# Kernel tuning notes

Hardware: AMD Instinct MI355X
Metric: run time of the kernel (lower is better)

Reference implementation:

```python
import jax, jax.numpy as jnp
import numpy as np

B, L, D, H = 4, 1024, 1024, 16
HD = D // H  # head_dim = 64


def setup_inputs() -> dict:
    key = jax.random.key(0)
    k1, k2, k3, k4 = jax.random.split(key, 4)
    x = jax.random.normal(k1, (B, L, D), dtype=jnp.float32)
    # causal mask: positions where mask == 0 are filled with -inf
    mask = jnp.tril(jnp.ones((L, L), dtype=bool))[None, None, :, :]  # [1,1,L,L]
    w_qkv = jax.random.normal(k2, (D, 3 * D), dtype=jnp.float32) * (D ** -0.5)
    w_out = jax.random.normal(k3, (D, D), dtype=jnp.float32) * (D ** -0.5)
    rel_pos_bias = jax.random.normal(k4, (H, L, L), dtype=jnp.float32) * 0.02
    return {"x": x, "mask": mask, "w_qkv": w_qkv, "w_out": w_out,
            "rel_pos_bias": rel_pos_bias}


def reference(x, mask, w_qkv, w_out, rel_pos_bias):
    b, l, d = x.shape
    scale = HD ** -0.5
    qkv = (x @ w_qkv).reshape(b, l, 3, H, HD)          # [B,L,3,H,hd]
    q, k, v = qkv[:, :, 0], qkv[:, :, 1], qkv[:, :, 2]  # each [B,L,H,hd]
    # scores: [B,H,Lq,Lk]
    scores = jnp.einsum('bqhd,bkhd->bhqk', q, k) * scale
    scores = scores + rel_pos_bias[None, :, :l, :l]
    scores = jnp.where(mask, scores, -jnp.inf)
    attn = jax.nn.softmax(scores, axis=-1)  # dropout is identity in eval
    out = jnp.einsum('bhqk,bkhd->bqhd', attn, v).reshape(b, l, d)
    return out @ w_out
```

## Files before the change

### kernel.cpp

```cpp
#include <hip/hip_runtime.h>
#include <hip/hip_bf16.h>
#include <math.h>

#define B_  4
#define L_  1024
#define D_  1024
#define H_  16
#define HD_ 64
#define SCALE 0.125f
#define LOG2E 1.44269504f
#define SCALE_L2E (0.125f * 1.44269504f)
#define NEG_BIG -3.0e38f

typedef __bf16 bf16x8 __attribute__((ext_vector_type(8)));
typedef float  f32x4  __attribute__((ext_vector_type(4)));

__device__ __forceinline__ float b2f(unsigned short u) {
    union { unsigned int i; float f; } x; x.i = ((unsigned)u) << 16; return x.f;
}
__device__ __forceinline__ unsigned short f2b(float f) {
    __hip_bfloat16 h = __float2bfloat16(f);
    return *reinterpret_cast<unsigned short*>(&h);
}
__device__ __forceinline__ void gl_lds16(const void* g, void* l) {
    __builtin_amdgcn_global_load_lds(
        (const __attribute__((address_space(1))) void*)g,
        (__attribute__((address_space(3))) void*)l, 16, 0, 0);
}

__global__ __launch_bounds__(256) void prep_kernel(
    const float* __restrict__ x, const float* __restrict__ w_qkv,
    const float* __restrict__ w_out, unsigned short* __restrict__ xb,
    unsigned short* __restrict__ wqkvT, unsigned short* __restrict__ woutT)
{
    const int bid = blockIdx.x;
    if (bid < 4096) {
        int i = (bid * 256 + threadIdx.x) * 4;
        float4 v = *(const float4*)&x[i];
        ushort4 o = make_ushort4(f2b(v.x), f2b(v.y), f2b(v.z), f2b(v.w));
        *(ushort4*)&xb[i] = o;
        return;
    }
    __shared__ float tile[32][33];
    const float* w; unsigned short* wt; int N, n0, k0;
    if (bid < 7168) {
        int b2 = bid - 4096;
        w = w_qkv; wt = wqkvT; N = 3072;
        n0 = (b2 % 96) * 32; k0 = (b2 / 96) * 32;
    } else {
        int b3 = bid - 7168;
        w = w_out; wt = woutT; N = 1024;
        n0 = (b3 % 32) * 32; k0 = (b3 / 32) * 32;
    }
    const int tx = threadIdx.x & 31, ty = threadIdx.x >> 5;
#pragma unroll
    for (int i = 0; i < 4; i++) {
        int kk = ty + i * 8;
        tile[kk][tx] = w[(size_t)(k0 + kk) * N + n0 + tx];
    }
    __syncthreads();
#pragma unroll
    for (int i = 0; i < 4; i++) {
        int nn = ty + i * 8;
        wt[(size_t)(n0 + nn) * 1024 + k0 + tx] = f2b(tile[tx][nn]);
    }
}

__device__ __forceinline__ void gemm_core(
    const unsigned short* __restrict__ A, const unsigned short* __restrict__ Bt,
    unsigned short* As, unsigned short* Bs,
    int m0, int n0, int wave, int lane, int wm, int wn,
    f32x4 acc[4][4])
{
    const int srow = lane >> 2, spos = lane & 3;
    const int sc   = spos ^ ((srow >> 1) & 3);
    const int mlane = lane & 15, chunk = lane >> 4;
    const int foff  = mlane * 32 + (chunk ^ ((mlane >> 1) & 3)) * 8;

    for (int k0 = 0; k0 < 1024; k0 += 32) {
#pragma unroll
        for (int t = 0; t < 2; t++) {
            int rb = wave * 32 + t * 16;
            int r  = rb + srow;
            gl_lds16(&A [(size_t)(m0 + r) * 1024 + k0 + sc * 8], &As[rb * 32]);
            gl_lds16(&Bt[(size_t)(n0 + r) * 1024 + k0 + sc * 8], &Bs[rb * 32]);
        }
        __syncthreads();
        bf16x8 af[4], bfr[4];
#pragma unroll
        for (int i = 0; i < 4; i++) {
            af[i]  = *(const bf16x8*)&As[(wm * 64 + i * 16) * 32 + foff];
            bfr[i] = *(const bf16x8*)&Bs[(wn * 64 + i * 16) * 32 + foff];
        }
#pragma unroll
        for (int i = 0; i < 4; i++)
#pragma unroll
            for (int j = 0; j < 4; j++)
                acc[i][j] = __builtin_amdgcn_mfma_f32_16x16x32_bf16(
                    bfr[i], af[j], acc[i][j], 0, 0, 0);
        __syncthreads();
    }
}

__global__ __launch_bounds__(256) void qkv_gemm_kernel(
    const unsigned short* __restrict__ A, const unsigned short* __restrict__ Bt,
    unsigned short* __restrict__ qb, unsigned short* __restrict__ kb,
    unsigned short* __restrict__ vtb)
{
    __shared__ unsigned short As[128 * 32];
    __shared__ unsigned short Bs[128 * 32];
    const int tid  = threadIdx.x;
    const int wave = tid >> 6, lane = tid & 63;
    const int quad = lane >> 4, l16 = lane & 15;
    const int wm = wave >> 1, wn = wave & 1;
    const int m0 = blockIdx.y * 128, n0 = blockIdx.x * 128;
    f32x4 acc[4][4] = {};
    gemm_core(A, Bt, As, Bs, m0, n0, wave, lane, wm, wn, acc);

    const int s = n0 >> 10;
#pragma unroll
    for (int i = 0; i < 4; i++) {
        int n_base = n0 + wn * 64 + i * 16 + quad * 4;
        int h = (n_base >> 6) & 15, hd0 = n_base & 63;
#pragma unroll
        for (int j = 0; j < 4; j++) {
            int m = m0 + wm * 64 + j * 16 + l16;
            int b = m >> 10, l = m & 1023;
            if (s == 2) {
#pragma unroll
                for (int r = 0; r < 4; r++)
                    vtb[((size_t)((b * 16 + h) * 64 + hd0 + r)) * 1024 + l] =
                        f2b(acc[i][j][r]);
            } else {
                unsigned short* dst = (s == 0) ? qb : kb;
                unsigned short tmp[4];
#pragma unroll
                for (int r = 0; r < 4; r++) tmp[r] = f2b(acc[i][j][r]);
                *(ushort4*)&dst[(((size_t)(b * 16 + h) * 1024 + l) << 6) + hd0] =
                    *(ushort4*)tmp;
            }
        }
    }
}

__global__ __launch_bounds__(256) void out_gemm_kernel(
    const unsigned short* __restrict__ A, const unsigned short* __restrict__ Bt,
    float* __restrict__ out)
{
    __shared__ unsigned short As[128 * 32];
    __shared__ unsigned short Bs[64 * 32];
    const int tid  = threadIdx.x;
    const int wave = tid >> 6, lane = tid & 63;
    const int quad = lane >> 4, l16 = lane & 15;
    const int srow = lane >> 2, spos = lane & 3;
    const int sc   = spos ^ ((srow >> 1) & 3);
    const int mlane = lane & 15, chunk = lane >> 4;
    const int foff  = mlane * 32 + (chunk ^ ((mlane >> 1) & 3)) * 8;
    const int m0 = blockIdx.y * 128, n0 = blockIdx.x * 64;
    f32x4 acc[4][2] = {};

    for (int k0 = 0; k0 < 1024; k0 += 32) {
#pragma unroll
        for (int t = 0; t < 2; t++) {
            int rb = wave * 32 + t * 16;
            gl_lds16(&A[(size_t)(m0 + rb + srow) * 1024 + k0 + sc * 8], &As[rb * 32]);
        }
        {
            int rb = wave * 16;
            gl_lds16(&Bt[(size_t)(n0 + rb + srow) * 1024 + k0 + sc * 8], &Bs[rb * 32]);
        }
        __syncthreads();
        bf16x8 af[2], bfr[4];
#pragma unroll
        for (int i = 0; i < 2; i++)
            af[i]  = *(const bf16x8*)&As[(wave * 32 + i * 16) * 32 + foff];
#pragma unroll
        for (int j = 0; j < 4; j++)
            bfr[j] = *(const bf16x8*)&Bs[(j * 16) * 32 + foff];
#pragma unroll
        for (int jn = 0; jn < 4; jn++)
#pragma unroll
            for (int im = 0; im < 2; im++)
                acc[jn][im] = __builtin_amdgcn_mfma_f32_16x16x32_bf16(
                    bfr[jn], af[im], acc[jn][im], 0, 0, 0);
        __syncthreads();
    }
#pragma unroll
    for (int jn = 0; jn < 4; jn++) {
        int n_base = n0 + jn * 16 + quad * 4;
#pragma unroll
        for (int im = 0; im < 2; im++) {
            int m = m0 + wave * 32 + im * 16 + l16;
            float4 o = make_float4(acc[jn][im][0], acc[jn][im][1],
                                   acc[jn][im][2], acc[jn][im][3]);
            *(float4*)&out[(size_t)m * 1024 + n_base] = o;
        }
    }
}

__global__ __launch_bounds__(256, 2) void attn_mfma_kernel(
    const unsigned short* __restrict__ qb, const unsigned short* __restrict__ kb,
    const unsigned short* __restrict__ vtb, const float* __restrict__ bias,
    unsigned short* __restrict__ ob)
{
    __shared__ unsigned short Ks [2 * 64 * 72];
    __shared__ unsigned short Vts[2 * 64 * 72];
    __shared__ unsigned short Ps [128 * 72];

    const int tid  = threadIdx.x;
    const int wave = tid >> 6, lane = tid & 63;
    const int quad = lane >> 4, l16 = lane & 15;
    const int bh = blockIdx.x, b = bh >> 4, h = bh & 15;
    const int jlo = blockIdx.y;
    const int jhi = 15 - jlo;
    const int ktmax = jhi;
    const int srow = tid >> 3, scol = (tid & 7) * 8;
    const size_t qkv_base = (size_t)bh * (1024 * 64);

    const int qH  = jhi * 64 + wave * 16;
    const int qL  = jlo * 64 + wave * 16;
    const int qgH = qH + quad * 4;
    const int qgL = qL + quad * 4;

    bf16x8 aH0 = *(const bf16x8*)&qb[qkv_base + (size_t)(qH + l16) * 64 + quad * 8];
    bf16x8 aH1 = *(const bf16x8*)&qb[qkv_base + (size_t)(qH + l16) * 64 + 32 + quad * 8];
    bf16x8 aL0 = *(const bf16x8*)&qb[qkv_base + (size_t)(qL + l16) * 64 + quad * 8];
    bf16x8 aL1 = *(const bf16x8*)&qb[qkv_base + (size_t)(qL + l16) * 64 + 32 + quad * 8];

    uint4 kpre0 = *(const uint4*)&kb [qkv_base + (size_t)srow * 64 + scol];
    uint4 kpre1 = *(const uint4*)&kb [qkv_base + (size_t)(srow + 32) * 64 + scol];
    uint4 vpre0 = *(const uint4*)&vtb[qkv_base + (size_t)srow * 1024 + scol];
    uint4 vpre1 = *(const uint4*)&vtb[qkv_base + (size_t)(srow + 32) * 1024 + scol];

    float bA[16], bB[16];
#pragma unroll
    for (int nt = 0; nt < 4; nt++)
#pragma unroll
        for (int r = 0; r < 4; r++)
            bA[nt * 4 + r] =
                bias[((size_t)h * 1024 + qgH + r) * 1024 + nt * 16 + l16] * LOG2E;

    float lrH[4] = {}, lrL[4] = {};
    f32x4 OH[4] = {}, OL[4] = {};

    *(uint4*)&Ks [srow * 72 + scol]        = kpre0;
    *(uint4*)&Ks [(srow + 32) * 72 + scol] = kpre1;
    *(uint4*)&Vts[srow * 72 + scol]        = vpre0;
    *(uint4*)&Vts[(srow + 32) * 72 + scol] = vpre1;
    __syncthreads();

    auto strip = [&](int kt, const bf16x8& a0, const bf16x8& a1, const float* bc,
                     int qg, int psrow, f32x4* O, float* lr, bool dg) {
        const unsigned short* Kc = &Ks [(kt & 1) * 4608];
        const unsigned short* Vc = &Vts[(kt & 1) * 4608];
        f32x4 sacc[4] = {};
        __builtin_amdgcn_s_setprio(1);
#pragma unroll
        for (int nt = 0; nt < 4; nt++) {
            bf16x8 k0 = *(const bf16x8*)&Kc[(nt * 16 + l16) * 72 + quad * 8];
            bf16x8 k1 = *(const bf16x8*)&Kc[(nt * 16 + l16) * 72 + 32 + quad * 8];
            sacc[nt] = __builtin_amdgcn_mfma_f32_16x16x32_bf16(a0, k0, sacc[nt], 0, 0, 0);
            sacc[nt] = __builtin_amdgcn_mfma_f32_16x16x32_bf16(a1, k1, sacc[nt], 0, 0, 0);
        }
        __builtin_amdgcn_s_setprio(0);
#pragma unroll
        for (int nt = 0; nt < 4; nt++) {
            const int kg = kt * 64 + nt * 16 + l16;
#pragma unroll
            for (int r = 0; r < 4; r++) {
                float v = fmaf(sacc[nt][r], SCALE_L2E, bc[nt * 4 + r]);
                if (dg && kg > qg + r) v = NEG_BIG;
                float p = exp2f(v);
                lr[r] += p;
                Ps[(psrow + quad * 4 + r) * 72 + nt * 16 + l16] = f2b(p);
            }
        }
        bf16x8 p0 = *(const bf16x8*)&Ps[(psrow + l16) * 72 + quad * 8];
        bf16x8 p1 = *(const bf16x8*)&Ps[(psrow + l16) * 72 + 32 + quad * 8];
        __builtin_amdgcn_s_setprio(1);
#pragma unroll
        for (int dt = 0; dt < 4; dt++) {
            bf16x8 v0 = *(const bf16x8*)&Vc[(dt * 16 + l16) * 72 + quad * 8];
            bf16x8 v1 = *(const bf16x8*)&Vc[(dt * 16 + l16) * 72 + 32 + quad * 8];
            O[dt] = __builtin_amdgcn_mfma_f32_16x16x32_bf16(p0, v0, O[dt], 0, 0, 0);
            O[dt] = __builtin_amdgcn_mfma_f32_16x16x32_bf16(p1, v1, O[dt], 0, 0, 0);
        }
        __builtin_amdgcn_s_setprio(0);
    };

    auto tile = [&](int kt, float* bc, float* bn) {
        const bool pf = (kt < ktmax);
        if (pf) {
            const int kn = (kt + 1) * 64;
            kpre0 = *(const uint4*)&kb [qkv_base + (size_t)(kn + srow) * 64 + scol];
            kpre1 = *(const uint4*)&kb [qkv_base + (size_t)(kn + srow + 32) * 64 + scol];
            vpre0 = *(const uint4*)&vtb[qkv_base + (size_t)srow * 1024 + kn + scol];
            vpre1 = *(const uint4*)&vtb[qkv_base + (size_t)(srow + 32) * 1024 + kn + scol];
            const float* bp = &bias[((size_t)h * 1024 + qgH) * 1024 + kn];
#pragma unroll
            for (int nt = 0; nt < 4; nt++)
#pragma unroll
                for (int r = 0; r < 4; r++)
                    bn[nt * 4 + r] = bp[(size_t)r * 1024 + nt * 16 + l16] * LOG2E;
        }
        const bool dolo = (kt <= jlo);
        float bl[16];
        if (dolo) {
            const float* bp = &bias[((size_t)h * 1024 + qgL) * 1024 + kt * 64];
#pragma unroll
            for (int nt = 0; nt < 4; nt++)
#pragma unroll
                for (int r = 0; r < 4; r++)
                    bl[nt * 4 + r] = bp[(size_t)r * 1024 + nt * 16 + l16] * LOG2E;
        }
        strip(kt, aH0, aH1, bc, qgH, wave * 32,      OH, lrH, kt == ktmax);
        if (dolo)
            strip(kt, aL0, aL1, bl, qgL, wave * 32 + 16, OL, lrL, kt == jlo);
        if (pf) {
            unsigned short* Kn = &Ks [((kt + 1) & 1) * 4608];
            unsigned short* Vn = &Vts[((kt + 1) & 1) * 4608];
            *(uint4*)&Kn[srow * 72 + scol]        = kpre0;
            *(uint4*)&Kn[(srow + 32) * 72 + scol] = kpre1;
            *(uint4*)&Vn[srow * 72 + scol]        = vpre0;
            *(uint4*)&Vn[(srow + 32) * 72 + scol] = vpre1;
        }
        __syncthreads();
    };

    for (int kt = 0; kt <= ktmax; kt += 2) {
        tile(kt, bA, bB);
        if (kt + 1 <= ktmax) tile(kt + 1, bB, bA);
    }

#pragma unroll
    for (int r = 0; r < 4; r++) {
        float s = lrH[r];
        s += __shfl_xor(s, 1); s += __shfl_xor(s, 2);
        s += __shfl_xor(s, 4); s += __shfl_xor(s, 8);
        float inv = 1.0f / s;
        int qg = qgH + r;
#pragma unroll
        for (int dt = 0; dt < 4; dt++)
            ob[((size_t)(b * 1024 + qg)) * 1024 + h * 64 + dt * 16 + l16] =
                f2b(OH[dt][r] * inv);
    }
#pragma unroll
    for (int r = 0; r < 4; r++) {
        float s = lrL[r];
        s += __shfl_xor(s, 1); s += __shfl_xor(s, 2);
        s += __shfl_xor(s, 4); s += __shfl_xor(s, 8);
        float inv = 1.0f / s;
        int qg = qgL + r;
#pragma unroll
        for (int dt = 0; dt < 4; dt++)
            ob[((size_t)(b * 1024 + qg)) * 1024 + h * 64 + dt * 16 + l16] =
                f2b(OL[dt][r] * inv);
    }
}


extern "C" void kernel_launch(void* const* d_in, const int* in_sizes, int n_in,
                              void* d_out, int out_size, void* d_ws, size_t ws_size,
                              hipStream_t stream) {
    const float* x     = (const float*)d_in[0];
    const float* w_qkv = (const float*)d_in[2];
    const float* w_out = (const float*)d_in[3];
    const float* bias  = (const float*)d_in[4];
    float* out = (float*)d_out;

    char* ws = (char*)d_ws;
    unsigned short* xb     = (unsigned short*)ws;              ws += (size_t)4096 * 1024 * 2;
    unsigned short* wqkvT  = (unsigned short*)ws;              ws += (size_t)3072 * 1024 * 2;
    unsigned short* woutT  = (unsigned short*)ws;              ws += (size_t)1024 * 1024 * 2;
    unsigned short* qb     = (unsigned short*)ws;              ws += (size_t)4096 * 1024 * 2;
    unsigned short* kb     = (unsigned short*)ws;              ws += (size_t)4096 * 1024 * 2;
    unsigned short* vtb    = (unsigned short*)ws;              ws += (size_t)4096 * 1024 * 2;
    unsigned short* ab     = (unsigned short*)ws;

    prep_kernel<<<8192, 256, 0, stream>>>(x, w_qkv, w_out, xb, wqkvT, woutT);
    qkv_gemm_kernel<<<dim3(24, 32), 256, 0, stream>>>(xb, wqkvT, qb, kb, vtb);
    attn_mfma_kernel<<<dim3(64, 8), 256, 0, stream>>>(qb, kb, vtb, bias, ab);
    out_gemm_kernel<<<dim3(16, 32), 256, 0, stream>>>(ab, woutT, out);
}
```

Before: 215.9 us.

## Drop paired causal q-tiles; one q-tile per block with more blocks and occupancy

Each attention block previously handled a high and a low query tile, pairing them to balance causal work. Now each block handles a single 64-row query tile, the grid doubles to 16 tiles per head, the P staging buffer halves, and launch bounds ask for 4 blocks per CU. The aim is more parallelism and occupancy, with less register pressure and LDS per block. The cost is uneven block lengths: the shortest tile does 1 key step and the longest 16. Blocks are launched longest-first to soften that imbalance, and each K/V tile load is now shared by one query tile instead of two.

```diff
diff --git a/kernel.cpp b/kernel.cpp
--- a/kernel.cpp
+++ b/kernel.cpp
@@ -198,34 +198,29 @@
     }
 }
 
-__global__ __launch_bounds__(256, 2) void attn_mfma_kernel(
+__global__ __launch_bounds__(256, 4) void attn_mfma_kernel(
     const unsigned short* __restrict__ qb, const unsigned short* __restrict__ kb,
     const unsigned short* __restrict__ vtb, const float* __restrict__ bias,
     unsigned short* __restrict__ ob)
 {
     __shared__ unsigned short Ks [2 * 64 * 72];
     __shared__ unsigned short Vts[2 * 64 * 72];
-    __shared__ unsigned short Ps [128 * 72];
+    __shared__ unsigned short Ps [64 * 72];
 
     const int tid  = threadIdx.x;
     const int wave = tid >> 6, lane = tid & 63;
     const int quad = lane >> 4, l16 = lane & 15;
     const int bh = blockIdx.x, b = bh >> 4, h = bh & 15;
-    const int jlo = blockIdx.y;
-    const int jhi = 15 - jlo;
-    const int ktmax = jhi;
+    const int qt = 15 - blockIdx.y;
+    const int q0 = qt * 64;
     const int srow = tid >> 3, scol = (tid & 7) * 8;
     const size_t qkv_base = (size_t)bh * (1024 * 64);
 
-    const int qH  = jhi * 64 + wave * 16;
-    const int qL  = jlo * 64 + wave * 16;
-    const int qgH = qH + quad * 4;
-    const int qgL = qL + quad * 4;
-
-    bf16x8 aH0 = *(const bf16x8*)&qb[qkv_base + (size_t)(qH + l16) * 64 + quad * 8];
-    bf16x8 aH1 = *(const bf16x8*)&qb[qkv_base + (size_t)(qH + l16) * 64 + 32 + quad * 8];
-    bf16x8 aL0 = *(const bf16x8*)&qb[qkv_base + (size_t)(qL + l16) * 64 + quad * 8];
-    bf16x8 aL1 = *(const bf16x8*)&qb[qkv_base + (size_t)(qL + l16) * 64 + 32 + quad * 8];
+    const int qrow = q0 + wave * 16;
+    const int qg   = qrow + quad * 4;
+
+    bf16x8 a0 = *(const bf16x8*)&qb[qkv_base + (size_t)(qrow + l16) * 64 + quad * 8];
+    bf16x8 a1 = *(const bf16x8*)&qb[qkv_base + (size_t)(qrow + l16) * 64 + 32 + quad * 8];
 
     uint4 kpre0 = *(const uint4*)&kb [qkv_base + (size_t)srow * 64 + scol];
     uint4 kpre1 = *(const uint4*)&kb [qkv_base + (size_t)(srow + 32) * 64 + scol];
@@ -238,10 +233,10 @@
 #pragma unroll
         for (int r = 0; r < 4; r++)
             bA[nt * 4 + r] =
-                bias[((size_t)h * 1024 + qgH + r) * 1024 + nt * 16 + l16] * LOG2E;
-
-    float lrH[4] = {}, lrL[4] = {};
-    f32x4 OH[4] = {}, OL[4] = {};
+                bias[((size_t)h * 1024 + qg + r) * 1024 + nt * 16 + l16] * LOG2E;
+
+    float lr[4] = {};
+    f32x4 O[4] = {};
 
     *(uint4*)&Ks [srow * 72 + scol]        = kpre0;
     *(uint4*)&Ks [(srow + 32) * 72 + scol] = kpre1;
@@ -249,73 +244,57 @@
     *(uint4*)&Vts[(srow + 32) * 72 + scol] = vpre1;
     __syncthreads();
 
-    auto strip = [&](int kt, const bf16x8& a0, const bf16x8& a1, const float* bc,
-                     int qg, int psrow, f32x4* O, float* lr, bool dg) {
-        const unsigned short* Kc = &Ks [(kt & 1) * 4608];
-        const unsigned short* Vc = &Vts[(kt & 1) * 4608];
-        f32x4 sacc[4] = {};
-        __builtin_amdgcn_s_setprio(1);
-#pragma unroll
-        for (int nt = 0; nt < 4; nt++) {
-            bf16x8 k0 = *(const bf16x8*)&Kc[(nt * 16 + l16) * 72 + quad * 8];
-            bf16x8 k1 = *(const bf16x8*)&Kc[(nt * 16 + l16) * 72 + 32 + quad * 8];
-            sacc[nt] = __builtin_amdgcn_mfma_f32_16x16x32_bf16(a0, k0, sacc[nt], 0, 0, 0);
-            sacc[nt] = __builtin_amdgcn_mfma_f32_16x16x32_bf16(a1, k1, sacc[nt], 0, 0, 0);
-        }
-        __builtin_amdgcn_s_setprio(0);
-#pragma unroll
-        for (int nt = 0; nt < 4; nt++) {
-            const int kg = kt * 64 + nt * 16 + l16;
-#pragma unroll
-            for (int r = 0; r < 4; r++) {
-                float v = fmaf(sacc[nt][r], SCALE_L2E, bc[nt * 4 + r]);
-                if (dg && kg > qg + r) v = NEG_BIG;
-                float p = exp2f(v);
-                lr[r] += p;
-                Ps[(psrow + quad * 4 + r) * 72 + nt * 16 + l16] = f2b(p);
-            }
-        }
-        bf16x8 p0 = *(const bf16x8*)&Ps[(psrow + l16) * 72 + quad * 8];
-        bf16x8 p1 = *(const bf16x8*)&Ps[(psrow + l16) * 72 + 32 + quad * 8];
-        __builtin_amdgcn_s_setprio(1);
-#pragma unroll
-        for (int dt = 0; dt < 4; dt++) {
-            bf16x8 v0 = *(const bf16x8*)&Vc[(dt * 16 + l16) * 72 + quad * 8];
-            bf16x8 v1 = *(const bf16x8*)&Vc[(dt * 16 + l16) * 72 + 32 + quad * 8];
-            O[dt] = __builtin_amdgcn_mfma_f32_16x16x32_bf16(p0, v0, O[dt], 0, 0, 0);
-            O[dt] = __builtin_amdgcn_mfma_f32_16x16x32_bf16(p1, v1, O[dt], 0, 0, 0);
-        }
-        __builtin_amdgcn_s_setprio(0);
-    };
-
     auto tile = [&](int kt, float* bc, float* bn) {
-        const bool pf = (kt < ktmax);
+        const bool pf = (kt < qt);
         if (pf) {
             const int kn = (kt + 1) * 64;
             kpre0 = *(const uint4*)&kb [qkv_base + (size_t)(kn + srow) * 64 + scol];
             kpre1 = *(const uint4*)&kb [qkv_base + (size_t)(kn + srow + 32) * 64 + scol];
             vpre0 = *(const uint4*)&vtb[qkv_base + (size_t)srow * 1024 + kn + scol];
             vpre1 = *(const uint4*)&vtb[qkv_base + (size_t)(srow + 32) * 1024 + kn + scol];
-            const float* bp = &bias[((size_t)h * 1024 + qgH) * 1024 + kn];
+            const float* bp = &bias[((size_t)h * 1024 + qg) * 1024 + kn];
 #pragma unroll
             for (int nt = 0; nt < 4; nt++)
 #pragma unroll
                 for (int r = 0; r < 4; r++)
                     bn[nt * 4 + r] = bp[(size_t)r * 1024 + nt * 16 + l16] * LOG2E;
         }
-        const bool dolo = (kt <= jlo);
-        float bl[16];
-        if (dolo) {
-            const float* bp = &bias[((size_t)h * 1024 + qgL) * 1024 + kt * 64];
-#pragma unroll
-            for (int nt = 0; nt < 4; nt++)
-#pragma unroll
-                for (int r = 0; r < 4; r++)
-                    bl[nt * 4 + r] = bp[(size_t)r * 1024 + nt * 16 + l16] * LOG2E;
-        }
-        strip(kt, aH0, aH1, bc, qgH, wave * 32,      OH, lrH, kt == ktmax);
-        if (dolo)
-            strip(kt, aL0, aL1, bl, qgL, wave * 32 + 16, OL, lrL, kt == jlo);
+        const unsigned short* Kc = &Ks [(kt & 1) * 4608];
+        const unsigned short* Vc = &Vts[(kt & 1) * 4608];
+        f32x4 sacc[4] = {};
+        __builtin_amdgcn_s_setprio(1);
+#pragma unroll
+        for (int nt = 0; nt < 4; nt++) {
+            bf16x8 k0 = *(const bf16x8*)&Kc[(nt * 16 + l16) * 72 + quad * 8];
+            bf16x8 k1 = *(const bf16x8*)&Kc[(nt * 16 + l16) * 72 + 32 + quad * 8];
+            sacc[nt] = __builtin_amdgcn_mfma_f32_16x16x32_bf16(a0, k0, sacc[nt], 0, 0, 0);
+            sacc[nt] = __builtin_amdgcn_mfma_f32_16x16x32_bf16(a1, k1, sacc[nt], 0, 0, 0);
+        }
+        __builtin_amdgcn_s_setprio(0);
+        const bool dg = (kt == qt);
+#pragma unroll
+        for (int nt = 0; nt < 4; nt++) {
+            const int kg = kt * 64 + nt * 16 + l16;
+#pragma unroll
+            for (int r = 0; r < 4; r++) {
+                float v = fmaf(sacc[nt][r], SCALE_L2E, bc[nt * 4 + r]);
+                if (dg && kg > qg + r) v = NEG_BIG;
+                float p = exp2f(v);
+                lr[r] += p;
+                Ps[(wave * 16 + quad * 4 + r) * 72 + nt * 16 + l16] = f2b(p);
+            }
+        }
+        bf16x8 p0 = *(const bf16x8*)&Ps[(wave * 16 + l16) * 72 + quad * 8];
+        bf16x8 p1 = *(const bf16x8*)&Ps[(wave * 16 + l16) * 72 + 32 + quad * 8];
+        __builtin_amdgcn_s_setprio(1);
+#pragma unroll
+        for (int dt = 0; dt < 4; dt++) {
+            bf16x8 v0 = *(const bf16x8*)&Vc[(dt * 16 + l16) * 72 + quad * 8];
+            bf16x8 v1 = *(const bf16x8*)&Vc[(dt * 16 + l16) * 72 + 32 + quad * 8];
+            O[dt] = __builtin_amdgcn_mfma_f32_16x16x32_bf16(p0, v0, O[dt], 0, 0, 0);
+            O[dt] = __builtin_amdgcn_mfma_f32_16x16x32_bf16(p1, v1, O[dt], 0, 0, 0);
+        }
+        __builtin_amdgcn_s_setprio(0);
         if (pf) {
             unsigned short* Kn = &Ks [((kt + 1) & 1) * 4608];
             unsigned short* Vn = &Vts[((kt + 1) & 1) * 4608];
@@ -327,34 +306,22 @@
         __syncthreads();
     };
 
-    for (int kt = 0; kt <= ktmax; kt += 2) {
+    for (int kt = 0; kt <= qt; kt += 2) {
         tile(kt, bA, bB);
-        if (kt + 1 <= ktmax) tile(kt + 1, bB, bA);
+        if (kt + 1 <= qt) tile(kt + 1, bB, bA);
     }
 
 #pragma unroll
     for (int r = 0; r < 4; r++) {
-        float s = lrH[r];
+        float s = lr[r];
         s += __shfl_xor(s, 1); s += __shfl_xor(s, 2);
         s += __shfl_xor(s, 4); s += __shfl_xor(s, 8);
         float inv = 1.0f / s;
-        int qg = qgH + r;
+        int qgr = qg + r;
 #pragma unroll
         for (int dt = 0; dt < 4; dt++)
-            ob[((size_t)(b * 1024 + qg)) * 1024 + h * 64 + dt * 16 + l16] =
-                f2b(OH[dt][r] * inv);
-    }
-#pragma unroll
-    for (int r = 0; r < 4; r++) {
-        float s = lrL[r];
-        s += __shfl_xor(s, 1); s += __shfl_xor(s, 2);
-        s += __shfl_xor(s, 4); s += __shfl_xor(s, 8);
-        float inv = 1.0f / s;
-        int qg = qgL + r;
-#pragma unroll
-        for (int dt = 0; dt < 4; dt++)
-            ob[((size_t)(b * 1024 + qg)) * 1024 + h * 64 + dt * 16 + l16] =
-                f2b(OL[dt][r] * inv);
+            ob[((size_t)(b * 1024 + qgr)) * 1024 + h * 64 + dt * 16 + l16] =
+                f2b(O[dt][r] * inv);
     }
 }
 
@@ -379,6 +346,6 @@
 
     prep_kernel<<<8192, 256, 0, stream>>>(x, w_qkv, w_out, xb, wqkvT, woutT);
     qkv_gemm_kernel<<<dim3(24, 32), 256, 0, stream>>>(xb, wqkvT, qb, kb, vtb);
-    attn_mfma_kernel<<<dim3(64, 8), 256, 0, stream>>>(qb, kb, vtb, bias, ab);
+    attn_mfma_kernel<<<dim3(64, 16), 256, 0, stream>>>(qb, kb, vtb, bias, ab);
     out_gemm_kernel<<<dim3(16, 32), 256, 0, stream>>>(ab, woutT, out);
 }
```

Result: no change. 215.5 us (-0.2%).
